# Kernel optimization log

Hardware: AMD Instinct MI355X
Metric: run time of the kernel (lower is better)

The kernel has to match this reference:

```python
import jax, jax.numpy as jnp
import numpy as np

DT = 1.0          # integration timestep (ms)
SIGMA = 0.5       # gauss_std for surrogate (unused in pure fwd spike)
AMPLITUDE = 0.3   # dampening_factor
N = 50000         # neurons
R = 4             # receptor types
D = 5             # max_delay
E = 5000000       # recurrent synapses
B = 4             # batch


def setup_inputs() -> dict:
    key = jax.random.key(0)
    ks = jax.random.split(key, 20)
    f = jnp.float32
    inputs = jax.random.normal(ks[0], (B, N * R), f) * 0.1
    # z_buf holds binary spikes for the last D steps
    z_buf = jax.random.bernoulli(ks[1], 0.05, (B, N * D)).astype(f)
    v = jax.random.uniform(ks[2], (B, N), f, 0.0, 1.0)
    r = jnp.zeros((B, N), f)
    asc_1 = jax.random.normal(ks[3], (B, N), f)
    asc_2 = jax.random.normal(ks[4], (B, N), f)
    psc_rise = jax.random.normal(ks[5], (B, N * R), f) * 0.5
    psc = jax.random.normal(ks[6], (B, N * R), f)
    rec_w = jax.random.normal(ks[7], (E,), f) * 0.01
    rec_rows = jax.random.randint(ks[8], (E,), 0, N * R, jnp.int32)
    rec_cols = jax.random.randint(ks[9], (E,), 0, N * D, jnp.int32)
    syn_decay = jax.random.uniform(ks[10], (N, R), f, 0.5, 0.99)
    psc_initial = jax.random.uniform(ks[11], (N, R), f, 0.1, 1.0)
    t_ref = jax.random.uniform(ks[12], (N,), f, 1.0, 4.0)
    asc_amps = jax.random.normal(ks[13], (N, 2), f)
    k = jax.random.normal(ks[14], (N, 2), f)  # inv-sigmoid space, read via sigmoid
    v_th = jnp.ones((N,), f)
    e_l = jnp.zeros((N,), f)
    v_reset = jnp.zeros((N,), f)
    g = jax.random.uniform(ks[15], (N,), f, 0.1, 1.0)
    decay = jax.random.uniform(ks[16], (N,), f, 0.8, 0.99)
    current_factor = jax.random.uniform(ks[17], (N,), f, 0.1, 1.0)
    voltage_scale = jnp.ones((N,), f) * 20.0
    voltage_offset = jnp.ones((N,), f) * -70.0
    return dict(inputs=inputs, z_buf=z_buf, v=v, r=r, asc_1=asc_1, asc_2=asc_2,
                psc_rise=psc_rise, psc=psc, rec_w=rec_w, rec_rows=rec_rows,
                rec_cols=rec_cols, syn_decay=syn_decay, psc_initial=psc_initial,
                t_ref=t_ref, asc_amps=asc_amps, k=k, v_th=v_th, e_l=e_l,
                v_reset=v_reset, g=g, decay=decay, current_factor=current_factor,
                voltage_scale=voltage_scale, voltage_offset=voltage_offset)


def _step(inputs, z_buf, v, r, asc_1, asc_2, psc_rise, psc,
          rec_w, rec_rows, rec_cols, syn_decay, psc_initial, t_ref,
          asc_amps, k, v_th, e_l, v_reset, g, decay, current_factor,
          voltage_scale, voltage_offset):
    shaped_z_buf = z_buf.reshape(B, D, N)
    prev_z = shaped_z_buf[:, 0]                      # most recent spikes [B,N]
    psc_rise_r = psc_rise.reshape(B, N, R)
    psc_r = psc.reshape(B, N, R)

    # sparse recurrent matmul: W[N*R, N*D] @ z_buf^T -> [N*R, B]
    vals = rec_w[:, None] * z_buf.T[rec_cols]        # [E, B] gather
    i_rec = jax.ops.segment_sum(vals, rec_rows, num_segments=N * R).T  # [B, N*R]

    rec_inputs = (i_rec + inputs).reshape(B, N, R)
    new_psc_rise = syn_decay * psc_rise_r + rec_inputs * psc_initial
    new_psc = psc_r * syn_decay + DT * syn_decay * psc_rise_r

    new_r = jax.nn.relu(r + prev_z * t_ref - DT)

    kk = jax.nn.sigmoid(k)                           # param_k_read()
    new_asc_1 = jnp.exp(-DT * kk[:, 0]) * asc_1 + prev_z * asc_amps[:, 0]
    new_asc_2 = jnp.exp(-DT * kk[:, 1]) * asc_2 + prev_z * asc_amps[:, 1]

    reset_current = prev_z * (v_reset - v_th)
    input_current = psc_r.sum(-1)                    # old psc
    c1 = input_current + asc_1 + asc_2 + g * e_l
    new_v = decay * v + current_factor * c1 + reset_current

    v_sc = (new_v - v_th) / (v_th - e_l)
    new_z = (v_sc > 0.0).astype(v_sc.dtype)          # spike_gauss forward
    new_z = jnp.where(new_r > 0.0, jnp.zeros_like(new_z), new_z)

    new_z_buf = jnp.concatenate([new_z[:, None], shaped_z_buf[:, :-1]], axis=1)
    out_v = new_v * voltage_scale + voltage_offset
    return (new_z, out_v, new_r, new_asc_1, new_asc_2,
            new_psc_rise.reshape(B, N * R), new_psc.reshape(B, N * R),
            new_z_buf.reshape(B, N * D))


def reference(inputs, z_buf, v, r, asc_1, asc_2, psc_rise, psc,
              rec_w, rec_rows, rec_cols, syn_decay, psc_initial, t_ref,
              asc_amps, k, v_th, e_l, v_reset, g, decay, current_factor,
              voltage_scale, voltage_offset):
    outs = _step(inputs, z_buf, v, r, asc_1, asc_2, psc_rise, psc,
                 rec_w, rec_rows, rec_cols, syn_decay, psc_initial, t_ref,
                 asc_amps, k, v_th, e_l, v_reset, g, decay, current_factor,
                 voltage_scale, voltage_offset)
    # pack outputs + new state into one [B, N*(5+2R+D)] array
    return jnp.concatenate(outs, axis=-1)
```

## Files before the change

kernel.cpp:

```cpp
#include <hip/hip_runtime.h>

#define Nn 50000
#define Rr 4
#define Dd 5
#define Ee 5000000
#define Bb 4
#define NRr (Nn * Rr)
#define NDd (Nn * Dd)

struct P {
    const float* inputs; const float* z_buf; const float* v; const float* r;
    const float* asc1; const float* asc2; const float* psc_rise; const float* psc;
    const float* rec_w; const int* rec_rows; const int* rec_cols;
    const float* syn_decay; const float* psc_initial; const float* t_ref;
    const float* asc_amps; const float* k; const float* v_th; const float* e_l;
    const float* v_reset; const float* g; const float* decay;
    const float* current_factor; const float* vscale; const float* voffset;
    float* out; unsigned char* z_pack;
};

__global__ __launch_bounds__(256) void pack_base_kernel(P p) {
    int i = blockIdx.x * 256 + threadIdx.x;
    if (i < NDd) {
        unsigned m = 0;
#pragma unroll
        for (int b = 0; b < Bb; ++b)
            if (p.z_buf[(size_t)b * NDd + i] != 0.0f) m |= (1u << b);
        p.z_pack[i] = (unsigned char)m;
    }
    if (i < Bb * Nn) {
        int b = i / Nn;
        int n = i - b * Nn;
        const size_t bnr = (size_t)b * NRr + (size_t)n * 4;
        float4 pr  = *(const float4*)(p.psc_rise + bnr);
        float4 in4 = *(const float4*)(p.inputs + bnr);
        float4 sd  = *(const float4*)(p.syn_decay + (size_t)n * 4);
        float4 pi  = *(const float4*)(p.psc_initial + (size_t)n * 4);
        float4 base;
        base.x = sd.x * pr.x + in4.x * pi.x;
        base.y = sd.y * pr.y + in4.y * pi.y;
        base.z = sd.z * pr.z + in4.z * pi.z;
        base.w = sd.w * pr.w + in4.w * pi.w;
        float* ob = p.out + (size_t)b * 18 * Nn;
        *(float4*)(ob + 5 * Nn + (size_t)n * 4) = base;
    }
}

__global__ __launch_bounds__(256) void edge_neuron_kernel(P p) {
    const int tid = blockIdx.x * 256 + threadIdx.x;

    if (tid < Bb * Nn) {
        int b = tid / Nn;
        int n = tid - b * Nn;
        const size_t bn  = (size_t)b * Nn + n;
        const size_t bnr = (size_t)b * NRr + (size_t)n * 4;

        float prev_z = p.z_buf[(size_t)b * NDd + n];
        float4 pr = *(const float4*)(p.psc_rise + bnr);
        float4 pc = *(const float4*)(p.psc + bnr);
        float4 sd = *(const float4*)(p.syn_decay + (size_t)n * 4);

        float4 npc;
        npc.x = pc.x * sd.x + sd.x * pr.x;
        npc.y = pc.y * sd.y + sd.y * pr.y;
        npc.z = pc.z * sd.z + sd.z * pr.z;
        npc.w = pc.w * sd.w + sd.w * pr.w;
        float input_current = pc.x + pc.y + pc.z + pc.w;

        float new_r = fmaxf(p.r[bn] + prev_z * p.t_ref[n] - 1.0f, 0.0f);

        float2 kv = *(const float2*)(p.k + (size_t)n * 2);
        float2 aa = *(const float2*)(p.asc_amps + (size_t)n * 2);
        float kk0 = 1.0f / (1.0f + expf(-kv.x));
        float kk1 = 1.0f / (1.0f + expf(-kv.y));
        float a1 = p.asc1[bn];
        float a2 = p.asc2[bn];
        float na1 = expf(-kk0) * a1 + prev_z * aa.x;
        float na2 = expf(-kk1) * a2 + prev_z * aa.y;

        float vth = p.v_th[n];
        float el  = p.e_l[n];
        float reset_current = prev_z * (p.v_reset[n] - vth);
        float c1 = input_current + a1 + a2 + p.g[n] * el;
        float new_v = p.decay[n] * p.v[bn] + p.current_factor[n] * c1
                      + reset_current;
        float v_sc = (new_v - vth) / (vth - el);
        float new_z = (v_sc > 0.0f) ? 1.0f : 0.0f;
        if (new_r > 0.0f) new_z = 0.0f;
        float out_v = new_v * p.vscale[n] + p.voffset[n];

        float* ob = p.out + (size_t)b * 18 * Nn;
        ob[n]          = new_z;
        ob[Nn + n]     = out_v;
        ob[2 * Nn + n] = new_r;
        ob[3 * Nn + n] = na1;
        ob[4 * Nn + n] = na2;
        *(float4*)(ob + 9 * Nn + (size_t)n * 4) = npc;
        ob[13 * Nn + n] = new_z;
#pragma unroll
        for (int d = 0; d < Dd - 1; ++d)
            ob[14 * Nn + (size_t)d * Nn + n] =
                p.z_buf[(size_t)b * NDd + (size_t)d * Nn + n];
    }

    if (tid < Ee / 4) {
        int4 c = ((const int4*)p.rec_cols)[tid];
        unsigned m0 = p.z_pack[c.x];
        unsigned m1 = p.z_pack[c.y];
        unsigned m2 = p.z_pack[c.z];
        unsigned m3 = p.z_pack[c.w];
        if (m0 | m1 | m2 | m3) {
            int4 rw = ((const int4*)p.rec_rows)[tid];
            float4 w = ((const float4*)p.rec_w)[tid];
            float* out5 = p.out + 5 * Nn;
            auto do_edge = [&](unsigned mm, int row, float wv) {
                if (mm) {
                    float s = wv * p.psc_initial[row];
                    float* o = out5 + row;
                    if (mm & 1u) atomicAdd(o, s);
                    if (mm & 2u) atomicAdd(o + 18 * Nn, s);
                    if (mm & 4u) atomicAdd(o + 36 * Nn, s);
                    if (mm & 8u) atomicAdd(o + 54 * Nn, s);
                }
            };
            do_edge(m0, rw.x, w.x);
            do_edge(m1, rw.y, w.y);
            do_edge(m2, rw.z, w.z);
            do_edge(m3, rw.w, w.w);
        }
    }
}

extern "C" void kernel_launch(void* const* d_in, const int* in_sizes, int n_in,
                              void* d_out, int out_size, void* d_ws, size_t ws_size,
                              hipStream_t stream) {
    P p;
    p.inputs        = (const float*)d_in[0];
    p.z_buf         = (const float*)d_in[1];
    p.v             = (const float*)d_in[2];
    p.r             = (const float*)d_in[3];
    p.asc1          = (const float*)d_in[4];
    p.asc2          = (const float*)d_in[5];
    p.psc_rise      = (const float*)d_in[6];
    p.psc           = (const float*)d_in[7];
    p.rec_w         = (const float*)d_in[8];
    p.rec_rows      = (const int*)d_in[9];
    p.rec_cols      = (const int*)d_in[10];
    p.syn_decay     = (const float*)d_in[11];
    p.psc_initial   = (const float*)d_in[12];
    p.t_ref         = (const float*)d_in[13];
    p.asc_amps      = (const float*)d_in[14];
    p.k             = (const float*)d_in[15];
    p.v_th          = (const float*)d_in[16];
    p.e_l           = (const float*)d_in[17];
    p.v_reset       = (const float*)d_in[18];
    p.g             = (const float*)d_in[19];
    p.decay         = (const float*)d_in[20];
    p.current_factor= (const float*)d_in[21];
    p.vscale        = (const float*)d_in[22];
    p.voffset       = (const float*)d_in[23];
    p.out           = (float*)d_out;
    p.z_pack = (unsigned char*)d_ws;

    pack_base_kernel<<<(NDd + 255) / 256, 256, 0, stream>>>(p);
    edge_neuron_kernel<<<(Ee / 4 + 255) / 256, 256, 0, stream>>>(p);
}
```

Before: 209.2 us.

## Stage any-batch spike bitmap in LDS and use persistent grid-stride edge loop

The pack kernel now also builds a 1-bit-per-presynaptic-slot 'any batch spiked' bitmap via wave ballot, which the edge kernel loads into shared memory (about 31 KB) so column lookups hit LDS instead of scattered global byte loads. The edge kernel becomes a persistent grid-stride loop over a fixed number of blocks, and the edge arrays are read with nontemporal loads. Per-batch masks are fetched from global only for edges whose source spiked. In exchange, every block pays the bitmap load and a sync, and the shared-memory footprint may lower occupancy.

```diff
diff --git a/kernel.cpp b/kernel.cpp
--- a/kernel.cpp
+++ b/kernel.cpp
@@ -7,6 +7,11 @@
 #define Bb 4
 #define NRr (Nn * Rr)
 #define NDd (Nn * Dd)
+#define ZW 7814
+#define PBLOCKS 1280
+
+typedef int   vi4 __attribute__((ext_vector_type(4)));
+typedef float vf4 __attribute__((ext_vector_type(4)));
 
 struct P {
     const float* inputs; const float* z_buf; const float* v; const float* r;
@@ -16,17 +21,22 @@
     const float* asc_amps; const float* k; const float* v_th; const float* e_l;
     const float* v_reset; const float* g; const float* decay;
     const float* current_factor; const float* vscale; const float* voffset;
-    float* out; unsigned char* z_pack;
+    float* out; unsigned char* z_pack; unsigned* zbits;
 };
 
 __global__ __launch_bounds__(256) void pack_base_kernel(P p) {
     int i = blockIdx.x * 256 + threadIdx.x;
+    unsigned m = 0;
     if (i < NDd) {
-        unsigned m = 0;
 #pragma unroll
         for (int b = 0; b < Bb; ++b)
             if (p.z_buf[(size_t)b * NDd + i] != 0.0f) m |= (1u << b);
         p.z_pack[i] = (unsigned char)m;
+    }
+    unsigned long long bal = __ballot(m != 0);
+    if ((i & 63) == 0 && i < NDd) {
+        p.zbits[(i >> 5)]     = (unsigned)bal;
+        p.zbits[(i >> 5) + 1] = (unsigned)(bal >> 32);
     }
     if (i < Bb * Nn) {
         int b = i / Nn;
@@ -47,9 +57,13 @@
 }
 
 __global__ __launch_bounds__(256) void edge_neuron_kernel(P p) {
-    const int tid = blockIdx.x * 256 + threadIdx.x;
+    __shared__ unsigned zb[ZW];
+    for (int t = threadIdx.x; t < ZW; t += 256) zb[t] = p.zbits[t];
+    __syncthreads();
+    const int gtid = blockIdx.x * 256 + threadIdx.x;
+    const int gsz  = gridDim.x * 256;
 
-    if (tid < Bb * Nn) {
+    for (int tid = gtid; tid < Bb * Nn; tid += gsz) {
         int b = tid / Nn;
         int n = tid - b * Nn;
         const size_t bn  = (size_t)b * Nn + n;
@@ -103,18 +117,19 @@
                 p.z_buf[(size_t)b * NDd + (size_t)d * Nn + n];
     }
 
-    if (tid < Ee / 4) {
-        int4 c = ((const int4*)p.rec_cols)[tid];
-        unsigned m0 = p.z_pack[c.x];
-        unsigned m1 = p.z_pack[c.y];
-        unsigned m2 = p.z_pack[c.z];
-        unsigned m3 = p.z_pack[c.w];
-        if (m0 | m1 | m2 | m3) {
-            int4 rw = ((const int4*)p.rec_rows)[tid];
-            float4 w = ((const float4*)p.rec_w)[tid];
+    for (int q = gtid; q < Ee / 4; q += gsz) {
+        vi4 c = __builtin_nontemporal_load((const vi4*)p.rec_cols + q);
+        unsigned h0 = (zb[(unsigned)c.x >> 5] >> (c.x & 31)) & 1u;
+        unsigned h1 = (zb[(unsigned)c.y >> 5] >> (c.y & 31)) & 1u;
+        unsigned h2 = (zb[(unsigned)c.z >> 5] >> (c.z & 31)) & 1u;
+        unsigned h3 = (zb[(unsigned)c.w >> 5] >> (c.w & 31)) & 1u;
+        if (h0 | h1 | h2 | h3) {
+            vi4 rw = __builtin_nontemporal_load((const vi4*)p.rec_rows + q);
+            vf4 w  = __builtin_nontemporal_load((const vf4*)p.rec_w + q);
             float* out5 = p.out + 5 * Nn;
-            auto do_edge = [&](unsigned mm, int row, float wv) {
-                if (mm) {
+            auto do_edge = [&](unsigned hh, int col, int row, float wv) {
+                if (hh) {
+                    unsigned mm = p.z_pack[col];
                     float s = wv * p.psc_initial[row];
                     float* o = out5 + row;
                     if (mm & 1u) atomicAdd(o, s);
@@ -123,10 +138,10 @@
                     if (mm & 8u) atomicAdd(o + 54 * Nn, s);
                 }
             };
-            do_edge(m0, rw.x, w.x);
-            do_edge(m1, rw.y, w.y);
-            do_edge(m2, rw.z, w.z);
-            do_edge(m3, rw.w, w.w);
+            do_edge(h0, c.x, rw.x, w.x);
+            do_edge(h1, c.y, rw.y, w.y);
+            do_edge(h2, c.z, rw.z, w.z);
+            do_edge(h3, c.w, rw.w, w.w);
         }
     }
 }
@@ -161,7 +176,8 @@
     p.voffset       = (const float*)d_in[23];
     p.out           = (float*)d_out;
     p.z_pack = (unsigned char*)d_ws;
+    p.zbits  = (unsigned*)((char*)d_ws + 256000);
 
     pack_base_kernel<<<(NDd + 255) / 256, 256, 0, stream>>>(p);
-    edge_neuron_kernel<<<(Ee / 4 + 255) / 256, 256, 0, stream>>>(p);
+    edge_neuron_kernel<<<PBLOCKS, 256, 0, stream>>>(p);
 }
```

Result: faster. 199.0 us (median of 2 runs) (-4.9%).
